# Optimization experiments

Measured on AMD Instinct MI355X. Metric: run time of the kernel, lower is better.

The kernel has to match this reference:

```python
import jax, jax.numpy as jnp
import numpy as np

HEAD_DIM = 64
SCALE = HEAD_DIM ** -0.5
NEG_INF = jnp.finfo(jnp.float32).min


def setup_inputs() -> dict:
    key = jax.random.key(0)
    kq, kk, kv = jax.random.split(key, 3)
    shape = (4, 16, 2048, HEAD_DIM)  # [batch, heads, seq, head_dim]
    return {
        "q": jax.random.normal(kq, shape, dtype=jnp.float32),
        "k": jax.random.normal(kk, shape, dtype=jnp.float32),
        "v": jax.random.normal(kv, shape, dtype=jnp.float32),
    }


def reference(q, k, v):
    # similarity = QK^T * scale, shape [b, h, i, j]
    sim = jnp.einsum("bhid,bhjd->bhij", q, k) * SCALE
    seq_len = sim.shape[-1]
    # causal mask: disallow j > i
    causal = jnp.triu(jnp.ones((seq_len, seq_len), dtype=bool), k=1)
    sim = jnp.where(causal, NEG_INF, sim)
    attn = jax.nn.softmax(sim, axis=-1)
    out = jnp.einsum("bhij,bhjd->bhid", attn, v)
    return out
```

## Files before the change

kernel.cpp:

```cpp
#include <hip/hip_runtime.h>
#include <hip/hip_bf16.h>

#define SEQ 2048
#define HD 64
#define NQB (SEQ / 128)

typedef __bf16 bf16x8 __attribute__((ext_vector_type(8)));
typedef float f32x4 __attribute__((ext_vector_type(4)));
typedef float f32x16 __attribute__((ext_vector_type(16)));
typedef unsigned int u32x4 __attribute__((ext_vector_type(4)));

typedef const __attribute__((address_space(1))) void gvoid_t;
typedef __attribute__((address_space(3))) void svoid_t;

__device__ __forceinline__ void gload_lds16(const void* g, void* l) {
  __builtin_amdgcn_global_load_lds((gvoid_t*)g, (svoid_t*)l, 16, 0, 0);
}

__device__ __forceinline__ bf16x8 cvt8(const float* p) {
  float4 a = *(const float4*)p;
  float4 b = *(const float4*)(p + 4);
  bf16x8 w;
  w[0] = (__bf16)a.x; w[1] = (__bf16)a.y; w[2] = (__bf16)a.z; w[3] = (__bf16)a.w;
  w[4] = (__bf16)b.x; w[5] = (__bf16)b.y; w[6] = (__bf16)b.z; w[7] = (__bf16)b.w;
  return w;
}

__device__ __forceinline__ unsigned cvtpk_bf16(float lo, float hi) {
  unsigned r;
  asm("v_cvt_pk_bf16_f32 %0, %1, %2" : "=v"(r) : "v"(lo), "v"(hi));
  return r;
}

__global__ void prep_kernel(const float* __restrict__ K,
                            const float* __restrict__ V,
                            unsigned short* __restrict__ Kswz,
                            unsigned short* __restrict__ Vt) {
  __shared__ __align__(16) unsigned short sT[64 * 72];
  const int t = threadIdx.x;
  const int kb = blockIdx.x;
  const int bh = blockIdx.y;
  const int j0 = kb * 64;
  const size_t ibase = (size_t)bh * SEQ * HD;

  {
    const int j = t >> 2;
    const int m = (t & 3) * 2;
    const float* src = K + ibase + (size_t)(j0 + j) * HD + m * 8;
    unsigned short* dst = Kswz + ibase + (size_t)(j0 + j) * HD;
#pragma unroll
    for (int h = 0; h < 2; ++h) {
      bf16x8 w = cvt8(src + 8 * h);
      const int c = (m + h) ^ (j & 7);
      *(bf16x8*)(dst + c * 8) = w;
    }
  }
  {
    const int jr = t >> 2;
    const int d0 = (t & 3) * 16;
    const float* vsrc = V + ibase + (size_t)(j0 + jr) * HD + d0;
#pragma unroll
    for (int h = 0; h < 4; ++h) {
      float4 a = *(const float4*)(vsrc + 4 * h);
      sT[(d0 + 4 * h + 0) * 72 + jr] = __builtin_bit_cast(unsigned short, (__bf16)a.x);
      sT[(d0 + 4 * h + 1) * 72 + jr] = __builtin_bit_cast(unsigned short, (__bf16)a.y);
      sT[(d0 + 4 * h + 2) * 72 + jr] = __builtin_bit_cast(unsigned short, (__bf16)a.z);
      sT[(d0 + 4 * h + 3) * 72 + jr] = __builtin_bit_cast(unsigned short, (__bf16)a.w);
    }
  }
  __syncthreads();
  {
#pragma unroll
    for (int p = 0; p < 2; ++p) {
      const int cid = t + 256 * p;
      const int d = cid >> 3;
      const int jj = cid & 7;
      bf16x8 w = *(const bf16x8*)(&sT[d * 72 + 8 * jj]);
      const int c = jj ^ (d & 7);
      *(bf16x8*)(Vt + (size_t)bh * HD * SEQ + (size_t)d * SEQ + j0 + c * 8) = w;
    }
  }
}

__global__ __launch_bounds__(256, 4) void fattn_kernel(
    const float* __restrict__ Q, const unsigned short* __restrict__ Kswz,
    const unsigned short* __restrict__ Vt, float* __restrict__ O) {
  __shared__ __align__(16) unsigned short sbuf[2][2 * 64 * 64];

  const int tid = threadIdx.x;
  const int wid = tid >> 6;
  const int lane = tid & 63;
  const int l31 = lane & 31;
  const int hi = lane >> 5;

  const int bh = blockIdx.y;
  const int cc0 = ((int)blockIdx.x + (bh >> 1)) & 15;
  const int qb = (cc0 < 8) ? (15 - cc0) : (cc0 - 8);

  const int i0w = qb * 128 + wid * 32;
  const int ig = i0w + l31;

  const float* Qp = Q + (size_t)bh * SEQ * HD;
  const unsigned short* Kg = Kswz + (size_t)bh * SEQ * HD;
  const unsigned short* Vg = Vt + (size_t)bh * HD * SEQ;
  float* Op = O + (size_t)bh * SEQ * HD;

  const float qscale = 0.125f * 1.44269504088896340736f;
  bf16x8 qf[4];
  {
    const float* qr = Qp + (size_t)ig * HD + 8 * hi;
#pragma unroll
    for (int c = 0; c < 4; ++c) {
      float4 a = *(const float4*)(qr + 16 * c);
      float4 b = *(const float4*)(qr + 16 * c + 4);
      bf16x8 w;
      w[0] = (__bf16)(a.x * qscale); w[1] = (__bf16)(a.y * qscale);
      w[2] = (__bf16)(a.z * qscale); w[3] = (__bf16)(a.w * qscale);
      w[4] = (__bf16)(b.x * qscale); w[5] = (__bf16)(b.y * qscale);
      w[6] = (__bf16)(b.z * qscale); w[7] = (__bf16)(b.w * qscale);
      qf[c] = w;
    }
  }

  f32x16 z16;
#pragma unroll
  for (int r = 0; r < 16; ++r) z16[r] = 0.f;

  f32x16 oA, oB;
#pragma unroll
  for (int r = 0; r < 16; ++r) { oA[r] = 0.f; oB[r] = 0.f; }
  float l_half = 0.f;

  const int nkb = 2 * qb + 2;

  auto stage = [&](int tile) {
    unsigned short* base = &sbuf[0][0] + (size_t)(tile & 1) * 8192;
    const int j0s = tile * 64;
#pragma unroll
    for (int tt = 0; tt < 2; ++tt) {
      const int row = 16 * wid + 8 * tt;
      const unsigned short* gk =
          Kg + (size_t)(j0s + row + (lane >> 3)) * HD + (lane & 7) * 8;
      gload_lds16(gk, base + row * HD);
      const unsigned short* gv =
          Vg + (size_t)(row + (lane >> 3)) * SEQ + j0s + (lane & 7) * 8;
      gload_lds16(gv, base + 4096 + row * HD);
    }
  };

  const int swz = (l31 & 7) << 4;

  stage(0);

  for (int kb = 0; kb < nkb; ++kb) {
    const int j0 = kb * 64;
    asm volatile("s_waitcnt vmcnt(0)" ::: "memory");
    __builtin_amdgcn_s_barrier();
    __builtin_amdgcn_sched_barrier(0);
    if (kb + 1 < nkb) stage(kb + 1);

    const unsigned short* base = &sbuf[0][0] + (size_t)(kb & 1) * 8192;
    const unsigned short* bK = base;
    const unsigned short* bV = base + 4096;

    f32x16 sA, sB;
    __builtin_amdgcn_s_setprio(1);
    {
      const int boff = (16 * hi) ^ swz;
      bf16x8 kf0 = *(const bf16x8*)((const char*)bK + l31 * 128 + boff);
      bf16x8 kf1 = *(const bf16x8*)((const char*)bK + (32 + l31) * 128 + boff);
      sA = __builtin_amdgcn_mfma_f32_32x32x16_bf16(kf0, qf[0], z16, 0, 0, 0);
      sB = __builtin_amdgcn_mfma_f32_32x32x16_bf16(kf1, qf[0], z16, 0, 0, 0);
    }
#pragma unroll
    for (int c = 1; c < 4; ++c) {
      const int boff = (32 * c + 16 * hi) ^ swz;
      bf16x8 kf0 = *(const bf16x8*)((const char*)bK + l31 * 128 + boff);
      bf16x8 kf1 = *(const bf16x8*)((const char*)bK + (32 + l31) * 128 + boff);
      sA = __builtin_amdgcn_mfma_f32_32x32x16_bf16(kf0, qf[c], sA, 0, 0, 0);
      sB = __builtin_amdgcn_mfma_f32_32x32x16_bf16(kf1, qf[c], sB, 0, 0, 0);
    }
    __builtin_amdgcn_s_setprio(0);

    if (j0 + 63 > i0w) {
#pragma unroll
      for (int r = 0; r < 16; ++r) {
        const int jl = j0 + (r & 3) + 8 * (r >> 2) + 4 * hi;
        sA[r] = (jl <= ig) ? sA[r] : -1e30f;
        sB[r] = (jl + 32 <= ig) ? sB[r] : -1e30f;
      }
    }

    bf16x8 pfr[4];
    {
      float rs0 = 0.f, rs1 = 0.f, rs2 = 0.f, rs3 = 0.f;
#pragma unroll
      for (int r = 0; r < 4; ++r) {
        sA[4 * r + 0] = __builtin_amdgcn_exp2f(sA[4 * r + 0]);
        sA[4 * r + 1] = __builtin_amdgcn_exp2f(sA[4 * r + 1]);
        sA[4 * r + 2] = __builtin_amdgcn_exp2f(sA[4 * r + 2]);
        sA[4 * r + 3] = __builtin_amdgcn_exp2f(sA[4 * r + 3]);
        rs0 += sA[4 * r + 0]; rs1 += sA[4 * r + 1];
        rs2 += sA[4 * r + 2]; rs3 += sA[4 * r + 3];
      }
#pragma unroll
      for (int r = 0; r < 4; ++r) {
        sB[4 * r + 0] = __builtin_amdgcn_exp2f(sB[4 * r + 0]);
        sB[4 * r + 1] = __builtin_amdgcn_exp2f(sB[4 * r + 1]);
        sB[4 * r + 2] = __builtin_amdgcn_exp2f(sB[4 * r + 2]);
        sB[4 * r + 3] = __builtin_amdgcn_exp2f(sB[4 * r + 3]);
        rs0 += sB[4 * r + 0]; rs1 += sB[4 * r + 1];
        rs2 += sB[4 * r + 2]; rs3 += sB[4 * r + 3];
      }
      l_half += (rs0 + rs1) + (rs2 + rs3);

#define MKFRAG(SV, BASE, DST)                                              \
      {                                                                    \
        unsigned a0 = cvtpk_bf16(SV[BASE + 0], SV[BASE + 1]);              \
        unsigned b0 = cvtpk_bf16(SV[BASE + 4], SV[BASE + 5]);              \
        asm("v_permlane32_swap_b32 %0, %1" : "+v"(a0), "+v"(b0));          \
        unsigned a1 = cvtpk_bf16(SV[BASE + 2], SV[BASE + 3]);              \
        unsigned b1 = cvtpk_bf16(SV[BASE + 6], SV[BASE + 7]);              \
        asm("v_permlane32_swap_b32 %0, %1" : "+v"(a1), "+v"(b1));          \
        u32x4 wv = {a0, a1, b0, b1};                                       \
        DST = __builtin_bit_cast(bf16x8, wv);                              \
      }
      MKFRAG(sA, 0, pfr[0])
      MKFRAG(sA, 8, pfr[1])
      MKFRAG(sB, 0, pfr[2])
      MKFRAG(sB, 8, pfr[3])
#undef MKFRAG
    }

    __builtin_amdgcn_s_setprio(1);
#pragma unroll
    for (int ks = 0; ks < 4; ++ks) {
      const int vbo = (32 * ks + 16 * hi) ^ swz;
      bf16x8 vf0 = *(const bf16x8*)((const char*)bV + l31 * 128 + vbo);
      bf16x8 vf1 = *(const bf16x8*)((const char*)bV + (32 + l31) * 128 + vbo);
      oA = __builtin_amdgcn_mfma_f32_32x32x16_bf16(vf0, pfr[ks], oA, 0, 0, 0);
      oB = __builtin_amdgcn_mfma_f32_32x32x16_bf16(vf1, pfr[ks], oB, 0, 0, 0);
    }
    __builtin_amdgcn_s_setprio(0);
  }

  const float l_tot = l_half + __shfl_xor(l_half, 32);
  const float inv = 1.f / l_tot;
  float* orow = Op + (size_t)ig * HD;
#pragma unroll
  for (int q2 = 0; q2 < 4; ++q2) {
    float4 o;
    o.x = oA[4 * q2 + 0] * inv; o.y = oA[4 * q2 + 1] * inv;
    o.z = oA[4 * q2 + 2] * inv; o.w = oA[4 * q2 + 3] * inv;
    *(float4*)(orow + 8 * q2 + 4 * hi) = o;
    float4 pq;
    pq.x = oB[4 * q2 + 0] * inv; pq.y = oB[4 * q2 + 1] * inv;
    pq.z = oB[4 * q2 + 2] * inv; pq.w = oB[4 * q2 + 3] * inv;
    *(float4*)(orow + 32 + 8 * q2 + 4 * hi) = pq;
  }
}

__global__ void fattn_fallback(const float* __restrict__ Q,
                               const float* __restrict__ K,
                               const float* __restrict__ V,
                               float* __restrict__ O) {
  __shared__ __align__(16) unsigned short sK[64 * 64];
  __shared__ __align__(16) unsigned short sVt[64 * 72];
  __shared__ __align__(16) unsigned short sP[4][16 * 72];

  const int tid = threadIdx.x;
  const int wid = tid >> 6;
  const int lane = tid & 63;
  const int g = lane >> 4;
  const int lx = lane & 15;

  const int qb = (int)gridDim.x - 1 - (int)blockIdx.x;
  const int bh = blockIdx.y;
  const int q0 = qb * 64;

  const size_t base = (size_t)bh * SEQ * HD;
  const float* Qp = Q + base;
  const float* Kp = K + base;
  const float* Vp = V + base;
  float* Op = O + base;

  bf16x8 qf[2];
  {
    const int row = q0 + wid * 16 + lx;
    const float* qr = Qp + (size_t)row * HD + 8 * g;
#pragma unroll
    for (int c = 0; c < 2; ++c) {
      float4 a = *(const float4*)(qr + 32 * c);
      float4 b = *(const float4*)(qr + 32 * c + 4);
      bf16x8 w;
      w[0] = (__bf16)(a.x * 0.125f); w[1] = (__bf16)(a.y * 0.125f);
      w[2] = (__bf16)(a.z * 0.125f); w[3] = (__bf16)(a.w * 0.125f);
      w[4] = (__bf16)(b.x * 0.125f); w[5] = (__bf16)(b.y * 0.125f);
      w[6] = (__bf16)(b.z * 0.125f); w[7] = (__bf16)(b.w * 0.125f);
      qf[c] = w;
    }
  }

  f32x4 acc[4];
#pragma unroll
  for (int dt = 0; dt < 4; ++dt) acc[dt] = (f32x4){0.f, 0.f, 0.f, 0.f};
  float m_run[4], l_run[4];
#pragma unroll
  for (int r = 0; r < 4; ++r) { m_run[r] = -1e30f; l_run[r] = 0.f; }

  const int iw0 = q0 + wid * 16;
  const int nkb = qb + 1;

  for (int kb = 0; kb < nkb; ++kb) {
    const int j0 = kb * 64;
    __syncthreads();
    {
      const int jr = tid >> 2;
      const int d0 = (tid & 3) * 16;
      const float* src = Kp + (size_t)(j0 + jr) * HD + d0;
#pragma unroll
      for (int h = 0; h < 2; ++h) {
        bf16x8 w = cvt8(src + 8 * h);
        const int byteoff = ((d0 + 8 * h) * 2) ^ ((jr & 7) << 4);
        *(bf16x8*)((char*)sK + jr * 128 + byteoff) = w;
      }
      const float* vsrc = Vp + (size_t)(j0 + jr) * HD + d0;
#pragma unroll
      for (int h = 0; h < 4; ++h) {
        float4 a = *(const float4*)(vsrc + 4 * h);
        sVt[(d0 + 4 * h + 0) * 72 + jr] = __builtin_bit_cast(unsigned short, (__bf16)a.x);
        sVt[(d0 + 4 * h + 1) * 72 + jr] = __builtin_bit_cast(unsigned short, (__bf16)a.y);
        sVt[(d0 + 4 * h + 2) * 72 + jr] = __builtin_bit_cast(unsigned short, (__bf16)a.z);
        sVt[(d0 + 4 * h + 3) * 72 + jr] = __builtin_bit_cast(unsigned short, (__bf16)a.w);
      }
    }
    __syncthreads();

    float s[4][4];
#pragma unroll
    for (int jt = 0; jt < 4; ++jt) {
      f32x4 c = (f32x4){0.f, 0.f, 0.f, 0.f};
#pragma unroll
      for (int cc = 0; cc < 2; ++cc) {
        const int row = jt * 16 + lx;
        const int byteoff = (16 * g + 64 * cc) ^ ((row & 7) << 4);
        bf16x8 kf = *(const bf16x8*)((const char*)sK + row * 128 + byteoff);
        c = __builtin_amdgcn_mfma_f32_16x16x32_bf16(qf[cc], kf, c, 0, 0, 0);
      }
      const int jg = j0 + jt * 16 + lx;
#pragma unroll
      for (int r = 0; r < 4; ++r) {
        const int igf = iw0 + 4 * g + r;
        s[jt][r] = (jg <= igf) ? c[r] : -1e30f;
      }
    }

#pragma unroll
    for (int r = 0; r < 4; ++r) {
      float mt = fmaxf(fmaxf(s[0][r], s[1][r]), fmaxf(s[2][r], s[3][r]));
#pragma unroll
      for (int msk = 1; msk <= 8; msk <<= 1) mt = fmaxf(mt, __shfl_xor(mt, msk));
      const float mn = fmaxf(m_run[r], mt);
      const float alpha = __expf(m_run[r] - mn);
      m_run[r] = mn;
      float rs = 0.f;
#pragma unroll
      for (int jt = 0; jt < 4; ++jt) {
        const float pv = __expf(s[jt][r] - mn);
        s[jt][r] = pv;
        rs += pv;
      }
#pragma unroll
      for (int msk = 1; msk <= 8; msk <<= 1) rs += __shfl_xor(rs, msk);
      l_run[r] = l_run[r] * alpha + rs;
#pragma unroll
      for (int dt = 0; dt < 4; ++dt) acc[dt][r] *= alpha;
    }

#pragma unroll
    for (int jt = 0; jt < 4; ++jt)
#pragma unroll
      for (int r = 0; r < 4; ++r)
        sP[wid][(4 * g + r) * 72 + jt * 16 + lx] =
            __builtin_bit_cast(unsigned short, (__bf16)s[jt][r]);
    asm volatile("s_waitcnt lgkmcnt(0)" ::: "memory");

#pragma unroll
    for (int cc = 0; cc < 2; ++cc) {
      bf16x8 pf = *(const bf16x8*)(&sP[wid][lx * 72 + 8 * g + 32 * cc]);
#pragma unroll
      for (int dt = 0; dt < 4; ++dt) {
        bf16x8 vf = *(const bf16x8*)(&sVt[(lx + 16 * dt) * 72 + 8 * g + 32 * cc]);
        acc[dt] = __builtin_amdgcn_mfma_f32_16x16x32_bf16(pf, vf, acc[dt], 0, 0, 0);
      }
    }
  }

#pragma unroll
  for (int r = 0; r < 4; ++r) {
    const float inv = 1.f / l_run[r];
    const int igf = q0 + wid * 16 + 4 * g + r;
    float* orow = Op + (size_t)igf * HD + lx;
#pragma unroll
    for (int dt = 0; dt < 4; ++dt) orow[16 * dt] = acc[dt][r] * inv;
  }
}

extern "C" void kernel_launch(void* const* d_in, const int* in_sizes, int n_in,
                              void* d_out, int out_size, void* d_ws, size_t ws_size,
                              hipStream_t stream) {
  const float* q = (const float*)d_in[0];
  const float* k = (const float*)d_in[1];
  const float* v = (const float*)d_in[2];
  float* o = (float*)d_out;

  const size_t kv_elems = (size_t)64 * SEQ * HD;
  const size_t need = 2 * kv_elems * sizeof(unsigned short);

  if (ws_size >= need) {
    unsigned short* kswz = (unsigned short*)d_ws;
    unsigned short* vt = kswz + kv_elems;
    dim3 pgrid(SEQ / 64, 64);
    prep_kernel<<<pgrid, 256, 0, stream>>>(k, v, kswz, vt);
    dim3 grid(NQB, 64);
    fattn_kernel<<<grid, 256, 0, stream>>>(q, kswz, vt, o);
  } else {
    dim3 grid(SEQ / 64, 64);
    fattn_fallback<<<grid, 256, 0, stream>>>(q, k, v, o);
  }
}
```

Before: 72.42 us.

## Load K/V MFMA fragments directly from global memory instead of LDS staging

Removes the double-buffered LDS staging of K and V tiles (global_load_lds, waitcnt, barriers) and has each lane load its bf16 MFMA operand fragments straight from global memory. The prep kernel no longer XOR-swizzles K and the transposed V, since there are no LDS bank conflicts left to avoid. This removes the per-tile barrier and LDS traffic but relies on L1/L2 to serve the K/V rows shared by the four waves. It also loses the explicit prefetch of the next tile, so global load latency is exposed inside the loop unless the compiler hoists loads. Setprio is now toggled per MFMA pair rather than around whole MFMA groups.

```diff
diff --git a/kernel.cpp b/kernel.cpp
--- a/kernel.cpp
+++ b/kernel.cpp
@@ -9,13 +9,6 @@
 typedef float f32x4 __attribute__((ext_vector_type(4)));
 typedef float f32x16 __attribute__((ext_vector_type(16)));
 typedef unsigned int u32x4 __attribute__((ext_vector_type(4)));
-
-typedef const __attribute__((address_space(1))) void gvoid_t;
-typedef __attribute__((address_space(3))) void svoid_t;
-
-__device__ __forceinline__ void gload_lds16(const void* g, void* l) {
-  __builtin_amdgcn_global_load_lds((gvoid_t*)g, (svoid_t*)l, 16, 0, 0);
-}
 
 __device__ __forceinline__ bf16x8 cvt8(const float* p) {
   float4 a = *(const float4*)p;
@@ -34,7 +27,7 @@
 
 __global__ void prep_kernel(const float* __restrict__ K,
                             const float* __restrict__ V,
-                            unsigned short* __restrict__ Kswz,
+                            unsigned short* __restrict__ Kb,
                             unsigned short* __restrict__ Vt) {
   __shared__ __align__(16) unsigned short sT[64 * 72];
   const int t = threadIdx.x;
@@ -47,12 +40,11 @@
     const int j = t >> 2;
     const int m = (t & 3) * 2;
     const float* src = K + ibase + (size_t)(j0 + j) * HD + m * 8;
-    unsigned short* dst = Kswz + ibase + (size_t)(j0 + j) * HD;
+    unsigned short* dst = Kb + ibase + (size_t)(j0 + j) * HD;
 #pragma unroll
     for (int h = 0; h < 2; ++h) {
       bf16x8 w = cvt8(src + 8 * h);
-      const int c = (m + h) ^ (j & 7);
-      *(bf16x8*)(dst + c * 8) = w;
+      *(bf16x8*)(dst + (m + h) * 8) = w;
     }
   }
   {
@@ -76,17 +68,14 @@
       const int d = cid >> 3;
       const int jj = cid & 7;
       bf16x8 w = *(const bf16x8*)(&sT[d * 72 + 8 * jj]);
-      const int c = jj ^ (d & 7);
-      *(bf16x8*)(Vt + (size_t)bh * HD * SEQ + (size_t)d * SEQ + j0 + c * 8) = w;
+      *(bf16x8*)(Vt + (size_t)bh * HD * SEQ + (size_t)d * SEQ + j0 + jj * 8) = w;
     }
   }
 }
 
 __global__ __launch_bounds__(256, 4) void fattn_kernel(
-    const float* __restrict__ Q, const unsigned short* __restrict__ Kswz,
+    const float* __restrict__ Q, const unsigned short* __restrict__ Kb,
     const unsigned short* __restrict__ Vt, float* __restrict__ O) {
-  __shared__ __align__(16) unsigned short sbuf[2][2 * 64 * 64];
-
   const int tid = threadIdx.x;
   const int wid = tid >> 6;
   const int lane = tid & 63;
@@ -101,7 +90,7 @@
   const int ig = i0w + l31;
 
   const float* Qp = Q + (size_t)bh * SEQ * HD;
-  const unsigned short* Kg = Kswz + (size_t)bh * SEQ * HD;
+  const unsigned short* Kg = Kb + (size_t)bh * SEQ * HD;
   const unsigned short* Vg = Vt + (size_t)bh * HD * SEQ;
   float* Op = O + (size_t)bh * SEQ * HD;
 
@@ -133,54 +122,32 @@
 
   const int nkb = 2 * qb + 2;
 
-  auto stage = [&](int tile) {
-    unsigned short* base = &sbuf[0][0] + (size_t)(tile & 1) * 8192;
-    const int j0s = tile * 64;
-#pragma unroll
-    for (int tt = 0; tt < 2; ++tt) {
-      const int row = 16 * wid + 8 * tt;
-      const unsigned short* gk =
-          Kg + (size_t)(j0s + row + (lane >> 3)) * HD + (lane & 7) * 8;
-      gload_lds16(gk, base + row * HD);
-      const unsigned short* gv =
-          Vg + (size_t)(row + (lane >> 3)) * SEQ + j0s + (lane & 7) * 8;
-      gload_lds16(gv, base + 4096 + row * HD);
-    }
-  };
-
-  const int swz = (l31 & 7) << 4;
-
-  stage(0);
+  const unsigned short* kRow0 = Kg + (size_t)l31 * HD + 8 * hi;
+  const unsigned short* kRow1 = Kg + (size_t)(32 + l31) * HD + 8 * hi;
+  const unsigned short* vRow0 = Vg + (size_t)l31 * SEQ + 8 * hi;
+  const unsigned short* vRow1 = Vg + (size_t)(32 + l31) * SEQ + 8 * hi;
 
   for (int kb = 0; kb < nkb; ++kb) {
     const int j0 = kb * 64;
-    asm volatile("s_waitcnt vmcnt(0)" ::: "memory");
-    __builtin_amdgcn_s_barrier();
-    __builtin_amdgcn_sched_barrier(0);
-    if (kb + 1 < nkb) stage(kb + 1);
-
-    const unsigned short* base = &sbuf[0][0] + (size_t)(kb & 1) * 8192;
-    const unsigned short* bK = base;
-    const unsigned short* bV = base + 4096;
 
     f32x16 sA, sB;
-    __builtin_amdgcn_s_setprio(1);
     {
-      const int boff = (16 * hi) ^ swz;
-      bf16x8 kf0 = *(const bf16x8*)((const char*)bK + l31 * 128 + boff);
-      bf16x8 kf1 = *(const bf16x8*)((const char*)bK + (32 + l31) * 128 + boff);
+      bf16x8 kf0 = *(const bf16x8*)(kRow0 + (size_t)j0 * HD);
+      bf16x8 kf1 = *(const bf16x8*)(kRow1 + (size_t)j0 * HD);
+      __builtin_amdgcn_s_setprio(1);
       sA = __builtin_amdgcn_mfma_f32_32x32x16_bf16(kf0, qf[0], z16, 0, 0, 0);
       sB = __builtin_amdgcn_mfma_f32_32x32x16_bf16(kf1, qf[0], z16, 0, 0, 0);
+      __builtin_amdgcn_s_setprio(0);
     }
 #pragma unroll
     for (int c = 1; c < 4; ++c) {
-      const int boff = (32 * c + 16 * hi) ^ swz;
-      bf16x8 kf0 = *(const bf16x8*)((const char*)bK + l31 * 128 + boff);
-      bf16x8 kf1 = *(const bf16x8*)((const char*)bK + (32 + l31) * 128 + boff);
+      bf16x8 kf0 = *(const bf16x8*)(kRow0 + (size_t)j0 * HD + 16 * c);
+      bf16x8 kf1 = *(const bf16x8*)(kRow1 + (size_t)j0 * HD + 16 * c);
+      __builtin_amdgcn_s_setprio(1);
       sA = __builtin_amdgcn_mfma_f32_32x32x16_bf16(kf0, qf[c], sA, 0, 0, 0);
       sB = __builtin_amdgcn_mfma_f32_32x32x16_bf16(kf1, qf[c], sB, 0, 0, 0);
-    }
-    __builtin_amdgcn_s_setprio(0);
+      __builtin_amdgcn_s_setprio(0);
+    }
 
     if (j0 + 63 > i0w) {
 #pragma unroll
@@ -232,16 +199,15 @@
 #undef MKFRAG
     }
 
-    __builtin_amdgcn_s_setprio(1);
 #pragma unroll
     for (int ks = 0; ks < 4; ++ks) {
-      const int vbo = (32 * ks + 16 * hi) ^ swz;
-      bf16x8 vf0 = *(const bf16x8*)((const char*)bV + l31 * 128 + vbo);
-      bf16x8 vf1 = *(const bf16x8*)((const char*)bV + (32 + l31) * 128 + vbo);
+      bf16x8 vf0 = *(const bf16x8*)(vRow0 + j0 + 16 * ks);
+      bf16x8 vf1 = *(const bf16x8*)(vRow1 + j0 + 16 * ks);
+      __builtin_amdgcn_s_setprio(1);
       oA = __builtin_amdgcn_mfma_f32_32x32x16_bf16(vf0, pfr[ks], oA, 0, 0, 0);
       oB = __builtin_amdgcn_mfma_f32_32x32x16_bf16(vf1, pfr[ks], oB, 0, 0, 0);
-    }
-    __builtin_amdgcn_s_setprio(0);
+      __builtin_amdgcn_s_setprio(0);
+    }
   }
 
   const float l_tot = l_half + __shfl_xor(l_half, 32);
@@ -418,12 +384,12 @@
   const size_t need = 2 * kv_elems * sizeof(unsigned short);
 
   if (ws_size >= need) {
-    unsigned short* kswz = (unsigned short*)d_ws;
-    unsigned short* vt = kswz + kv_elems;
+    unsigned short* kb = (unsigned short*)d_ws;
+    unsigned short* vt = kb + kv_elems;
     dim3 pgrid(SEQ / 64, 64);
-    prep_kernel<<<pgrid, 256, 0, stream>>>(k, v, kswz, vt);
+    prep_kernel<<<pgrid, 256, 0, stream>>>(k, v, kb, vt);
     dim3 grid(NQB, 64);
-    fattn_kernel<<<grid, 256, 0, stream>>>(q, kswz, vt, o);
+    fattn_kernel<<<grid, 256, 0, stream>>>(q, kb, vt, o);
   } else {
     dim3 grid(SEQ / 64, 64);
     fattn_fallback<<<grid, 256, 0, stream>>>(q, k, v, o);
```

Measured after the change: 152.7 us. +110.9%, slower.

## Split causal KV range across two blocks per query tile and add combine kernel

Applied to the files above, without the earlier changes.

Each query tile's key range is split into two halves processed by separate blocks, doubling the grid to improve occupancy and load balance. Unnormalized partial outputs and row sums are written to workspace and a separate combine kernel sums them and normalizes. This adds an extra kernel launch and substantial extra global memory traffic for the partial outputs, and only activates when the workspace is large enough.

```diff
diff --git a/kernel.cpp b/kernel.cpp
--- a/kernel.cpp
+++ b/kernel.cpp
@@ -82,9 +82,11 @@
   }
 }
 
-__global__ __launch_bounds__(256, 4) void fattn_kernel(
+__global__ __launch_bounds__(256, 4) void fattn_split(
     const float* __restrict__ Q, const unsigned short* __restrict__ Kswz,
-    const unsigned short* __restrict__ Vt, float* __restrict__ O) {
+    const unsigned short* __restrict__ Vt, float* __restrict__ Og,
+    float* __restrict__ part, float* __restrict__ l0buf,
+    float* __restrict__ l1buf) {
   __shared__ __align__(16) unsigned short sbuf[2][2 * 64 * 64];
 
   const int tid = threadIdx.x;
@@ -94,7 +96,8 @@
   const int hi = lane >> 5;
 
   const int bh = blockIdx.y;
-  const int cc0 = ((int)blockIdx.x + (bh >> 1)) & 15;
+  const int half = (int)blockIdx.x >> 4;
+  const int cc0 = (((int)blockIdx.x & 15) + (bh >> 1)) & 15;
   const int qb = (cc0 < 8) ? (15 - cc0) : (cc0 - 8);
 
   const int i0w = qb * 128 + wid * 32;
@@ -103,7 +106,6 @@
   const float* Qp = Q + (size_t)bh * SEQ * HD;
   const unsigned short* Kg = Kswz + (size_t)bh * SEQ * HD;
   const unsigned short* Vg = Vt + (size_t)bh * HD * SEQ;
-  float* Op = O + (size_t)bh * SEQ * HD;
 
   const float qscale = 0.125f * 1.44269504088896340736f;
   bf16x8 qf[4];
@@ -131,7 +133,8 @@
   for (int r = 0; r < 16; ++r) { oA[r] = 0.f; oB[r] = 0.f; }
   float l_half = 0.f;
 
-  const int nkb = 2 * qb + 2;
+  const int kb0 = half ? (qb + 1) : 0;
+  const int kbN = half ? (2 * qb + 2) : (qb + 1);
 
   auto stage = [&](int tile) {
     unsigned short* base = &sbuf[0][0] + (size_t)(tile & 1) * 8192;
@@ -150,14 +153,14 @@
 
   const int swz = (l31 & 7) << 4;
 
-  stage(0);
-
-  for (int kb = 0; kb < nkb; ++kb) {
+  stage(kb0);
+
+  for (int kb = kb0; kb < kbN; ++kb) {
     const int j0 = kb * 64;
     asm volatile("s_waitcnt vmcnt(0)" ::: "memory");
     __builtin_amdgcn_s_barrier();
     __builtin_amdgcn_sched_barrier(0);
-    if (kb + 1 < nkb) stage(kb + 1);
+    if (kb + 1 < kbN) stage(kb + 1);
 
     const unsigned short* base = &sbuf[0][0] + (size_t)(kb & 1) * 8192;
     const unsigned short* bK = base;
@@ -245,6 +248,202 @@
   }
 
   const float l_tot = l_half + __shfl_xor(l_half, 32);
+  float* dst = (half ? part : Og) + (size_t)bh * SEQ * HD + (size_t)ig * HD;
+  if (hi == 0) (half ? l1buf : l0buf)[(size_t)bh * SEQ + ig] = l_tot;
+#pragma unroll
+  for (int q2 = 0; q2 < 4; ++q2) {
+    float4 o;
+    o.x = oA[4 * q2 + 0]; o.y = oA[4 * q2 + 1];
+    o.z = oA[4 * q2 + 2]; o.w = oA[4 * q2 + 3];
+    *(float4*)(dst + 8 * q2 + 4 * hi) = o;
+    float4 pq;
+    pq.x = oB[4 * q2 + 0]; pq.y = oB[4 * q2 + 1];
+    pq.z = oB[4 * q2 + 2]; pq.w = oB[4 * q2 + 3];
+    *(float4*)(dst + 32 + 8 * q2 + 4 * hi) = pq;
+  }
+}
+
+__global__ void combine_kernel(float* __restrict__ O,
+                               const float* __restrict__ part,
+                               const float* __restrict__ l0,
+                               const float* __restrict__ l1) {
+  const size_t total4 = (size_t)64 * SEQ * HD / 4;
+  float4* O4 = (float4*)O;
+  const float4* P4 = (const float4*)part;
+  for (size_t i = blockIdx.x * blockDim.x + threadIdx.x; i < total4;
+       i += (size_t)gridDim.x * blockDim.x) {
+    const size_t row = i >> 4;
+    const float inv = 1.f / (l0[row] + l1[row]);
+    float4 a = O4[i], b = P4[i];
+    a.x = (a.x + b.x) * inv; a.y = (a.y + b.y) * inv;
+    a.z = (a.z + b.z) * inv; a.w = (a.w + b.w) * inv;
+    O4[i] = a;
+  }
+}
+
+__global__ __launch_bounds__(256, 4) void fattn_kernel(
+    const float* __restrict__ Q, const unsigned short* __restrict__ Kswz,
+    const unsigned short* __restrict__ Vt, float* __restrict__ O) {
+  __shared__ __align__(16) unsigned short sbuf[2][2 * 64 * 64];
+
+  const int tid = threadIdx.x;
+  const int wid = tid >> 6;
+  const int lane = tid & 63;
+  const int l31 = lane & 31;
+  const int hi = lane >> 5;
+
+  const int bh = blockIdx.y;
+  const int cc0 = ((int)blockIdx.x + (bh >> 1)) & 15;
+  const int qb = (cc0 < 8) ? (15 - cc0) : (cc0 - 8);
+
+  const int i0w = qb * 128 + wid * 32;
+  const int ig = i0w + l31;
+
+  const float* Qp = Q + (size_t)bh * SEQ * HD;
+  const unsigned short* Kg = Kswz + (size_t)bh * SEQ * HD;
+  const unsigned short* Vg = Vt + (size_t)bh * HD * SEQ;
+  float* Op = O + (size_t)bh * SEQ * HD;
+
+  const float qscale = 0.125f * 1.44269504088896340736f;
+  bf16x8 qf[4];
+  {
+    const float* qr = Qp + (size_t)ig * HD + 8 * hi;
+#pragma unroll
+    for (int c = 0; c < 4; ++c) {
+      float4 a = *(const float4*)(qr + 16 * c);
+      float4 b = *(const float4*)(qr + 16 * c + 4);
+      bf16x8 w;
+      w[0] = (__bf16)(a.x * qscale); w[1] = (__bf16)(a.y * qscale);
+      w[2] = (__bf16)(a.z * qscale); w[3] = (__bf16)(a.w * qscale);
+      w[4] = (__bf16)(b.x * qscale); w[5] = (__bf16)(b.y * qscale);
+      w[6] = (__bf16)(b.z * qscale); w[7] = (__bf16)(b.w * qscale);
+      qf[c] = w;
+    }
+  }
+
+  f32x16 z16;
+#pragma unroll
+  for (int r = 0; r < 16; ++r) z16[r] = 0.f;
+
+  f32x16 oA, oB;
+#pragma unroll
+  for (int r = 0; r < 16; ++r) { oA[r] = 0.f; oB[r] = 0.f; }
+  float l_half = 0.f;
+
+  const int nkb = 2 * qb + 2;
+
+  auto stage = [&](int tile) {
+    unsigned short* base = &sbuf[0][0] + (size_t)(tile & 1) * 8192;
+    const int j0s = tile * 64;
+#pragma unroll
+    for (int tt = 0; tt < 2; ++tt) {
+      const int row = 16 * wid + 8 * tt;
+      const unsigned short* gk =
+          Kg + (size_t)(j0s + row + (lane >> 3)) * HD + (lane & 7) * 8;
+      gload_lds16(gk, base + row * HD);
+      const unsigned short* gv =
+          Vg + (size_t)(row + (lane >> 3)) * SEQ + j0s + (lane & 7) * 8;
+      gload_lds16(gv, base + 4096 + row * HD);
+    }
+  };
+
+  const int swz = (l31 & 7) << 4;
+
+  stage(0);
+
+  for (int kb = 0; kb < nkb; ++kb) {
+    const int j0 = kb * 64;
+    asm volatile("s_waitcnt vmcnt(0)" ::: "memory");
+    __builtin_amdgcn_s_barrier();
+    __builtin_amdgcn_sched_barrier(0);
+    if (kb + 1 < nkb) stage(kb + 1);
+
+    const unsigned short* base = &sbuf[0][0] + (size_t)(kb & 1) * 8192;
+    const unsigned short* bK = base;
+    const unsigned short* bV = base + 4096;
+
+    f32x16 sA, sB;
+    __builtin_amdgcn_s_setprio(1);
+    {
+      const int boff = (16 * hi) ^ swz;
+      bf16x8 kf0 = *(const bf16x8*)((const char*)bK + l31 * 128 + boff);
+      bf16x8 kf1 = *(const bf16x8*)((const char*)bK + (32 + l31) * 128 + boff);
+      sA = __builtin_amdgcn_mfma_f32_32x32x16_bf16(kf0, qf[0], z16, 0, 0, 0);
+      sB = __builtin_amdgcn_mfma_f32_32x32x16_bf16(kf1, qf[0], z16, 0, 0, 0);
+    }
+#pragma unroll
+    for (int c = 1; c < 4; ++c) {
+      const int boff = (32 * c + 16 * hi) ^ swz;
+      bf16x8 kf0 = *(const bf16x8*)((const char*)bK + l31 * 128 + boff);
+      bf16x8 kf1 = *(const bf16x8*)((const char*)bK + (32 + l31) * 128 + boff);
+      sA = __builtin_amdgcn_mfma_f32_32x32x16_bf16(kf0, qf[c], sA, 0, 0, 0);
+      sB = __builtin_amdgcn_mfma_f32_32x32x16_bf16(kf1, qf[c], sB, 0, 0, 0);
+    }
+    __builtin_amdgcn_s_setprio(0);
+
+    if (j0 + 63 > i0w) {
+#pragma unroll
+      for (int r = 0; r < 16; ++r) {
+        const int jl = j0 + (r & 3) + 8 * (r >> 2) + 4 * hi;
+        sA[r] = (jl <= ig) ? sA[r] : -1e30f;
+        sB[r] = (jl + 32 <= ig) ? sB[r] : -1e30f;
+      }
+    }
+
+    bf16x8 pfr[4];
+    {
+      float rs0 = 0.f, rs1 = 0.f, rs2 = 0.f, rs3 = 0.f;
+#pragma unroll
+      for (int r = 0; r < 4; ++r) {
+        sA[4 * r + 0] = __builtin_amdgcn_exp2f(sA[4 * r + 0]);
+        sA[4 * r + 1] = __builtin_amdgcn_exp2f(sA[4 * r + 1]);
+        sA[4 * r + 2] = __builtin_amdgcn_exp2f(sA[4 * r + 2]);
+        sA[4 * r + 3] = __builtin_amdgcn_exp2f(sA[4 * r + 3]);
+        rs0 += sA[4 * r + 0]; rs1 += sA[4 * r + 1];
+        rs2 += sA[4 * r + 2]; rs3 += sA[4 * r + 3];
+      }
+#pragma unroll
+      for (int r = 0; r < 4; ++r) {
+        sB[4 * r + 0] = __builtin_amdgcn_exp2f(sB[4 * r + 0]);
+        sB[4 * r + 1] = __builtin_amdgcn_exp2f(sB[4 * r + 1]);
+        sB[4 * r + 2] = __builtin_amdgcn_exp2f(sB[4 * r + 2]);
+        sB[4 * r + 3] = __builtin_amdgcn_exp2f(sB[4 * r + 3]);
+        rs0 += sB[4 * r + 0]; rs1 += sB[4 * r + 1];
+        rs2 += sB[4 * r + 2]; rs3 += sB[4 * r + 3];
+      }
+      l_half += (rs0 + rs1) + (rs2 + rs3);
+
+#define MKFRAG(SV, BASE, DST)                                              \
+      {                                                                    \
+        unsigned a0 = cvtpk_bf16(SV[BASE + 0], SV[BASE + 1]);              \
+        unsigned b0 = cvtpk_bf16(SV[BASE + 4], SV[BASE + 5]);              \
+        asm("v_permlane32_swap_b32 %0, %1" : "+v"(a0), "+v"(b0));          \
+        unsigned a1 = cvtpk_bf16(SV[BASE + 2], SV[BASE + 3]);              \
+        unsigned b1 = cvtpk_bf16(SV[BASE + 6], SV[BASE + 7]);              \
+        asm("v_permlane32_swap_b32 %0, %1" : "+v"(a1), "+v"(b1));          \
+        u32x4 wv = {a0, a1, b0, b1};                                       \
+        DST = __builtin_bit_cast(bf16x8, wv);                              \
+      }
+      MKFRAG(sA, 0, pfr[0])
+      MKFRAG(sA, 8, pfr[1])
+      MKFRAG(sB, 0, pfr[2])
+      MKFRAG(sB, 8, pfr[3])
+#undef MKFRAG
+    }
+
+    __builtin_amdgcn_s_setprio(1);
+#pragma unroll
+    for (int ks = 0; ks < 4; ++ks) {
+      const int vbo = (32 * ks + 16 * hi) ^ swz;
+      bf16x8 vf0 = *(const bf16x8*)((const char*)bV + l31 * 128 + vbo);
+      bf16x8 vf1 = *(const bf16x8*)((const char*)bV + (32 + l31) * 128 + vbo);
+      oA = __builtin_amdgcn_mfma_f32_32x32x16_bf16(vf0, pfr[ks], oA, 0, 0, 0);
+      oB = __builtin_amdgcn_mfma_f32_32x32x16_bf16(vf1, pfr[ks], oB, 0, 0, 0);
+    }
+    __builtin_amdgcn_s_setprio(0);
+  }
+
+  const float l_tot = l_half + __shfl_xor(l_half, 32);
   const float inv = 1.f / l_tot;
   float* orow = Op + (size_t)ig * HD;
 #pragma unroll
@@ -415,9 +614,24 @@
   float* o = (float*)d_out;
 
   const size_t kv_elems = (size_t)64 * SEQ * HD;
-  const size_t need = 2 * kv_elems * sizeof(unsigned short);
-
-  if (ws_size >= need) {
+  const size_t kv_bytes = 2 * kv_elems * sizeof(unsigned short);
+  const size_t part_bytes = (size_t)64 * SEQ * HD * sizeof(float);
+  const size_t l_bytes = 2 * (size_t)64 * SEQ * sizeof(float);
+  const size_t need_split = kv_bytes + part_bytes + l_bytes;
+  const size_t need_r11 = kv_bytes;
+
+  if (ws_size >= need_split) {
+    unsigned short* kswz = (unsigned short*)d_ws;
+    unsigned short* vt = kswz + kv_elems;
+    float* part = (float*)((char*)d_ws + kv_bytes);
+    float* l0 = (float*)((char*)d_ws + kv_bytes + part_bytes);
+    float* l1 = l0 + (size_t)64 * SEQ;
+    dim3 pgrid(SEQ / 64, 64);
+    prep_kernel<<<pgrid, 256, 0, stream>>>(k, v, kswz, vt);
+    dim3 grid(2 * NQB, 64);
+    fattn_split<<<grid, 256, 0, stream>>>(q, kswz, vt, o, part, l0, l1);
+    combine_kernel<<<2048, 256, 0, stream>>>(o, part, l0, l1);
+  } else if (ws_size >= need_r11) {
     unsigned short* kswz = (unsigned short*)d_ws;
     unsigned short* vt = kswz + kv_elems;
     dim3 pgrid(SEQ / 64, 64);
```

Result: slower. 97.15 us (+34.1%).
